# Kernel tuning notes

Measured on AMD Instinct MI355X. Metric: run time of the kernel, lower is better.

Reference implementation:

```python
import jax, jax.numpy as jnp
import numpy as np

FEAT_STRIDE = 16
SCORE_THRESH = 0.7
DIST_THRESH = 16.0
MAX_OUT = 50
B = 2048
IMG_W = 65536


def setup_inputs() -> dict:
    key = jax.random.key(0)
    k1, k2, k3 = jax.random.split(key, 3)
    fw = IMG_W // FEAT_STRIDE
    pred_cls_logit = jax.random.normal(k1, (B, fw), dtype=jnp.float32)
    pred_delta = jax.random.normal(k2, (B, fw, 2), dtype=jnp.float32)
    # realistic image widths in [0.5, 1.0] * img_width
    real_images_width = jax.random.uniform(k3, (B,), jnp.float32, 0.5, 1.0) * IMG_W
    return {
        "pred_cls_logit": pred_cls_logit,
        "pred_delta": pred_delta,
        "img_width": IMG_W,
        "real_images_width": real_images_width,
    }


def _nms_one(positions, scores):
    # positions: [N, 2], scores: [N]. Greedy 1D NMS, fixed MAX_OUT iterations.
    centers = positions.mean(axis=1)                      # [N]
    alive0 = scores >= SCORE_THRESH                       # score-threshold filter

    def step(alive, _):
        masked = jnp.where(alive, scores, -1e30)
        i = jnp.argmax(masked)                            # highest remaining score
        has = jnp.any(alive)
        f = has.astype(jnp.float32)                       # 1.0 if a box was picked
        p = positions[i] * f
        s = scores[i] * f
        # suppress everything within DIST_THRESH of picked center (incl. itself)
        new_alive = alive & (jnp.abs(centers - centers[i]) > DIST_THRESH)
        return new_alive, (p, s, f)

    _, (P, S, F) = jax.lax.scan(step, alive0, None, length=MAX_OUT)
    # pad_to_fixed_size: append validity flag column, zero-padded rows
    nms_positions = jnp.concatenate([P, F[:, None]], axis=1)   # [MAX_OUT, 3]
    nms_scores = jnp.concatenate([S[:, None], F[:, None]], axis=1)  # [MAX_OUT, 2]
    return nms_positions, nms_scores


def reference(pred_cls_logit, pred_delta, img_width, real_images_width):
    feat_width = img_width // FEAT_STRIDE
    interval_center = (jnp.arange(feat_width, dtype=jnp.float32) + 0.5) * FEAT_STRIDE
    # [B, feat_width, 2]
    pos = pred_delta * FEAT_STRIDE + interval_center[None, :, None]
    scores = jax.nn.sigmoid(pred_cls_logit)               # [B, feat_width]
    max_width = real_images_width[:, None, None] - 1.0
    pos = jnp.where(pos < 0.0, 0.0, pos)
    pos = jnp.where(pos > max_width, max_width, pos)

    nms_positions, nms_scores = jax.vmap(_nms_one)(pos, scores)

    nms_center = nms_positions[..., :2].mean(axis=2)      # [B, MAX_OUT]
    x_interval_num = jnp.floor(nms_center / FEAT_STRIDE).astype(jnp.int32)
    valid = nms_positions[..., 2] == 1.0
    idx = jnp.where(valid, x_interval_num, feat_width)    # out-of-range -> dropped
    cls_ids = jax.vmap(
        lambda ii: jnp.zeros((feat_width,), jnp.float32).at[ii].set(1.0, mode='drop')
    )(idx)                                                # [B, feat_width]
    return nms_positions, nms_scores, cls_ids
```

## Files before the change

### kernel.cpp

```cpp
#include <hip/hip_runtime.h>
#include <math.h>

#define FW 4096
#define MAX_OUT 50
#define WCAP 320
#define NSLOT 1024


__global__ __launch_bounds__(256) void essp_k1(
    const float* __restrict__ logits,
    const float* __restrict__ deltas,
    const float* __restrict__ realw,
    float* stage)
{
  __shared__ float Lx[4][WCAP];
  __shared__ int   Li[4][WCAP];
  __shared__ int   Lcnt[4];

  const int row  = blockIdx.x;
  const int tid  = threadIdx.x;
  const int lane = tid & 63;
  const int w    = tid >> 6;

  const float mw = realw[row] - 1.0f;
  const float* lgr = logits + (size_t)row * FW;
  const float* dlr = deltas + (size_t)row * (2 * FW);

  int cnt = 0;
  #pragma unroll
  for (int r = 0; r < 4; ++r) {
    const int i0 = w * 1024 + r * 256 + 4 * lane;
    const float4 lx = *(const float4*)(lgr + i0);
    const float xs[4] = {lx.x, lx.y, lx.z, lx.w};
    bool c4[4]; unsigned long long m4[4];
    #pragma unroll
    for (int e = 0; e < 4; ++e) { c4[e] = (xs[e] >= 0.846f); m4[e] = __ballot(c4[e]); }
    const unsigned long long below = (1ULL << lane) - 1ULL;
    int base = cnt + __popcll(m4[0] & below) + __popcll(m4[1] & below)
                   + __popcll(m4[2] & below) + __popcll(m4[3] & below);
    int off = 0;
    #pragma unroll
    for (int e = 0; e < 4; ++e) {
      if (c4[e]) {
        const int slot = base + off;
        if (slot < WCAP) { Lx[w][slot] = xs[e]; Li[w][slot] = i0 + e; }
        ++off;
      }
    }
    cnt += __popcll(m4[0]) + __popcll(m4[1]) + __popcll(m4[2]) + __popcll(m4[3]);
  }
  if (lane == 0) Lcnt[w] = (cnt < WCAP) ? cnt : WCAP;
  __syncthreads();

  const int c0 = Lcnt[0], c1 = Lcnt[1], c2 = Lcnt[2], c3 = Lcnt[3];
  const int p1 = c0, p2 = c0 + c1, p3 = c0 + c1 + c2;
  int nc = p3 + c3; nc = (nc < NSLOT) ? nc : NSLOT;

  float* Srow = stage + (size_t)row * FW;
  unsigned short* idxrow = (unsigned short*)(Srow + 2048);

  #pragma unroll
  for (int g0 = 0; g0 < NSLOT; g0 += 256) {
    const int g = g0 + tid;
    float score = -1e30f, cen = 0.0f;
    int idx = 0;
    if (g < nc) {
      const int wsel = (g >= p1) + (g >= p2) + (g >= p3);
      int pre = 0;
      pre = (wsel == 1) ? p1 : pre;
      pre = (wsel == 2) ? p2 : pre;
      pre = (wsel == 3) ? p3 : pre;
      const int kk = g - pre;
      const float x = (&Lx[0][0])[wsel * WCAP + kk];
      idx = (&Li[0][0])[wsel * WCAP + kk];
      const float2 d = *(const float2*)(dlr + 2 * idx);
      const float ic = ((float)idx + 0.5f) * 16.0f;
      float q0 = d.x * 16.0f + ic;
      float q1 = d.y * 16.0f + ic;
      q0 = (q0 < 0.f) ? 0.f : q0;  q0 = (q0 > mw) ? mw : q0;
      q1 = (q1 < 0.f) ? 0.f : q1;  q1 = (q1 > mw) ? mw : q1;
      cen = (q0 + q1) * 0.5f;
      const float s = (float)(1.0 / (1.0 + exp(-(double)x)));
      score = (s >= 0.7f) ? s : -1e30f;
    }
    Srow[g]        = score;
    Srow[1024 + g] = cen;
    idxrow[g]      = (unsigned short)idx;
  }
}

#define INIT1(J, SS, CE, SLOT)                                                \
  unsigned long long k##J = ((SS) >= 0.7f)                                    \
      ? ((((unsigned long long)__float_as_uint(SS)) << 11)                    \
         | (unsigned)(2047 - (SLOT)))                                         \
      : 0ULL;                                                                 \
  const float c##J = (CE);

#define M2(RK, RC, KA, CA, KB, CB)                                            \
  const bool t##RK = (KB) > (KA);                                             \
  const unsigned long long RK = t##RK ? (KB) : (KA);                          \
  const float RC = t##RK ? (CB) : (CA);

#define BSTEP(CTRL) {                                                         \
  const unsigned lo_ = (unsigned)__builtin_amdgcn_update_dpp(                 \
      (int)(unsigned)bk, (int)(unsigned)bk, CTRL, 0xF, 0xF, false);           \
  const unsigned hi_ = (unsigned)__builtin_amdgcn_update_dpp(                 \
      (int)(unsigned)(bk >> 32), (int)(unsigned)(bk >> 32), CTRL, 0xF, 0xF,   \
      false);                                                                 \
  const float oc_ = __int_as_float(__builtin_amdgcn_update_dpp(               \
      __float_as_int(bc), __float_as_int(bc), CTRL, 0xF, 0xF, false));        \
  const unsigned long long ok_ = ((unsigned long long)hi_ << 32) | lo_;       \
  const bool tb_ = ok_ > bk;                                                  \
  bk = tb_ ? ok_ : bk;  bc = tb_ ? oc_ : bc; }

#define SUP(J) {                                                              \
  const bool ts_ = fabsf(c##J - wc) <= 16.0f;                                 \
  k##J = ts_ ? 0ULL : k##J; }

__global__ __launch_bounds__(64) void essp_k2(
    const float* __restrict__ deltas,
    const float* __restrict__ realw,
    float* out_pos,
    float* out_scr,
    float* cls_all)
{
  const int row  = blockIdx.x;
  const int lane = threadIdx.x;
  const int l4   = 4 * lane;
  float* Srow = cls_all + (size_t)row * FW;

  const float4 s4a = *(const float4*)(Srow + l4);
  const float4 s4b = *(const float4*)(Srow + 256 + l4);
  const float4 s4c = *(const float4*)(Srow + 512 + l4);
  const float4 s4d = *(const float4*)(Srow + 768 + l4);
  const float4 e4a = *(const float4*)(Srow + 1024 + l4);
  const float4 e4b = *(const float4*)(Srow + 1280 + l4);
  const float4 e4c = *(const float4*)(Srow + 1536 + l4);
  const float4 e4d = *(const float4*)(Srow + 1792 + l4);

  INIT1(0,  s4a.x, e4a.x, l4 + 0)
  INIT1(1,  s4a.y, e4a.y, l4 + 1)
  INIT1(2,  s4a.z, e4a.z, l4 + 2)
  INIT1(3,  s4a.w, e4a.w, l4 + 3)
  INIT1(4,  s4b.x, e4b.x, 256 + l4 + 0)
  INIT1(5,  s4b.y, e4b.y, 256 + l4 + 1)
  INIT1(6,  s4b.z, e4b.z, 256 + l4 + 2)
  INIT1(7,  s4b.w, e4b.w, 256 + l4 + 3)
  INIT1(8,  s4c.x, e4c.x, 512 + l4 + 0)
  INIT1(9,  s4c.y, e4c.y, 512 + l4 + 1)
  INIT1(10, s4c.z, e4c.z, 512 + l4 + 2)
  INIT1(11, s4c.w, e4c.w, 512 + l4 + 3)
  INIT1(12, s4d.x, e4d.x, 768 + l4 + 0)
  INIT1(13, s4d.y, e4d.y, 768 + l4 + 1)
  INIT1(14, s4d.z, e4d.z, 768 + l4 + 2)
  INIT1(15, s4d.w, e4d.w, 768 + l4 + 3)

  int pkv = -1;
  float psv = 0.f;

  #pragma unroll 1
  for (int it = 0; it < MAX_OUT; ++it) {
    M2(ka0, ca0, k0,  c0,  k1,  c1)
    M2(ka1, ca1, k2,  c2,  k3,  c3)
    M2(ka2, ca2, k4,  c4,  k5,  c5)
    M2(ka3, ca3, k6,  c6,  k7,  c7)
    M2(ka4, ca4, k8,  c8,  k9,  c9)
    M2(ka5, ca5, k10, c10, k11, c11)
    M2(ka6, ca6, k12, c12, k13, c13)
    M2(ka7, ca7, k14, c14, k15, c15)
    M2(kb0, cb0, ka0, ca0, ka1, ca1)
    M2(kb1, cb1, ka2, ca2, ka3, ca3)
    M2(kb2, cb2, ka4, ca4, ka5, ca5)
    M2(kb3, cb3, ka6, ca6, ka7, ca7)
    M2(kc0, cc0, kb0, cb0, kb1, cb1)
    M2(kc1, cc1, kb2, cb2, kb3, cb3)
    M2(kd0, cd0, kc0, cc0, kc1, cc1)

    unsigned long long bk = kd0;
    float bc = cd0;
    BSTEP(0xB1)
    BSTEP(0x4E)
    BSTEP(0x141)
    BSTEP(0x140)
    BSTEP(0x142)
    BSTEP(0x143)

    const unsigned rhi = (unsigned)__builtin_amdgcn_readlane(
        (int)(unsigned)(bk >> 32), 63);
    const unsigned rlo = (unsigned)__builtin_amdgcn_readlane(
        (int)(unsigned)bk, 63);
    const float rc = __int_as_float(
        __builtin_amdgcn_readlane(__float_as_int(bc), 63));

    const unsigned sbits = (rhi << 21) | (rlo >> 11);
    const bool valid = sbits != 0u;
    const float wc = valid ? rc : 3.0e38f;
    if (lane == it) {
      pkv = valid ? (2047 - (int)(rlo & 0x7FFu)) : -1;
      psv = __uint_as_float(sbits);
    }
    SUP(0)  SUP(1)  SUP(2)  SUP(3)  SUP(4)  SUP(5)  SUP(6)  SUP(7)
    SUP(8)  SUP(9)  SUP(10) SUP(11) SUP(12) SUP(13) SUP(14) SUP(15)
  }

  float p0 = 0.f, p1 = 0.f;
  int ci = -1;
  if (pkv >= 0) {
    const int idx = ((const unsigned short*)(Srow + 2048))[pkv];
    const float2 d = *(const float2*)(deltas + (size_t)row * (2 * FW) + 2 * idx);
    const float mw = realw[row] - 1.0f;
    const float ic = ((float)idx + 0.5f) * 16.0f;
    p0 = d.x * 16.0f + ic;
    p1 = d.y * 16.0f + ic;
    p0 = (p0 < 0.f) ? 0.f : p0;  p0 = (p0 > mw) ? mw : p0;
    p1 = (p1 < 0.f) ? 0.f : p1;  p1 = (p1 > mw) ? mw : p1;
    ci = (int)floorf(((p0 + p1) * 0.5f) * 0.0625f);
  }
  asm volatile("s_waitcnt vmcnt(0)" ::: "memory");

  const float4 z4 = make_float4(0.f, 0.f, 0.f, 0.f);
  #pragma unroll
  for (int q = 0; q < 16; ++q)
    *(float4*)(Srow + 256 * q + l4) = z4;
  asm volatile("s_waitcnt vmcnt(0)" ::: "memory");

  float* prow = out_pos + (size_t)row * (MAX_OUT * 3);
  float* srow = out_scr + (size_t)row * (MAX_OUT * 2);
  if (lane < MAX_OUT) {
    if (pkv >= 0) {
      prow[3 * lane + 0] = p0;
      prow[3 * lane + 1] = p1;
      prow[3 * lane + 2] = 1.0f;
      srow[2 * lane + 0] = psv;
      srow[2 * lane + 1] = 1.0f;
      if (ci >= 0 && ci < FW) Srow[ci] = 1.0f;
    } else {
      prow[3 * lane + 0] = 0.0f;
      prow[3 * lane + 1] = 0.0f;
      prow[3 * lane + 2] = 0.0f;
      srow[2 * lane + 0] = 0.0f;
      srow[2 * lane + 1] = 0.0f;
    }
  }
}

extern "C" void kernel_launch(void* const* d_in, const int* in_sizes, int n_in,
                              void* d_out, int out_size, void* d_ws, size_t ws_size,
                              hipStream_t stream) {
  const float* logits = (const float*)d_in[0];
  const float* deltas = (const float*)d_in[1];
  const float* realw  = (const float*)d_in[3];
  const int Bn = in_sizes[3];
  float* out_pos = (float*)d_out;
  float* out_scr = out_pos + (size_t)Bn * MAX_OUT * 3;
  float* out_cls = out_scr + (size_t)Bn * MAX_OUT * 2;

  essp_k1<<<Bn, 256, 0, stream>>>(logits, deltas, realw, out_cls);
  essp_k2<<<Bn, 64, 0, stream>>>(deltas, realw, out_pos, out_scr, out_cls);
}
```

Before: 64.02 us.

## Prefilter top candidates by threshold bisection, run NMS on one register per lane

Before greedy NMS, the kernel bisects on the score bits with ballot counts to find a threshold that keeps between 50 and 64 candidates. It compacts those into shared memory so each lane holds one key, which removes the 16-way per-lane reduction tree and the 16 suppress compares from each of the 50 iterations. If the top 64 run out before 50 picks, it falls back to the original full-register loop, and it also exits early when nothing is left alive. The bisection adds up to 34 ballot passes per row, and rows that hit the fallback pay for both paths.

```diff
diff --git a/kernel.cpp b/kernel.cpp
--- a/kernel.cpp
+++ b/kernel.cpp
@@ -89,12 +89,27 @@
   }
 }
 
-#define INIT1(J, SS, CE, SLOT)                                                \
-  unsigned long long k##J = ((SS) >= 0.7f)                                    \
-      ? ((((unsigned long long)__float_as_uint(SS)) << 11)                    \
-         | (unsigned)(2047 - (SLOT)))                                         \
-      : 0ULL;                                                                 \
+#define KDEF(J, SS, CE)                                                       \
+  const unsigned kb##J = ((SS) >= 0.7f) ? __float_as_uint(SS) : 0u;           \
   const float c##J = (CE);
+
+#define CNT1(J) cmid += __popcll(__ballot(kb##J >= mid));
+#define ALV1(J) alive += __popcll(__ballot(kb##J != 0u));
+
+#define CPT(J, SLOTEXPR) {                                                    \
+  const unsigned long long mm_ = __ballot(kb##J >= T);                        \
+  if (kb##J >= T) {                                                           \
+    const int pos_ = nsel + __popcll(mm_ & below);                            \
+    Lkey[pos_] = (((unsigned long long)kb##J) << 11)                          \
+                 | (unsigned)(2047 - (SLOTEXPR));                             \
+    Lcen[pos_] = c##J;                                                        \
+  }                                                                           \
+  nsel += __popcll(mm_); }
+
+#define INIT1F(J, SLOTEXPR)                                                   \
+  unsigned long long fk##J = kb##J                                            \
+      ? ((((unsigned long long)kb##J) << 11) | (unsigned)(2047 - (SLOTEXPR))) \
+      : 0ULL;
 
 #define M2(RK, RC, KA, CA, KB, CB)                                            \
   const bool t##RK = (KB) > (KA);                                             \
@@ -113,9 +128,9 @@
   const bool tb_ = ok_ > bk;                                                  \
   bk = tb_ ? ok_ : bk;  bc = tb_ ? oc_ : bc; }
 
-#define SUP(J) {                                                              \
+#define SUPF(J) {                                                             \
   const bool ts_ = fabsf(c##J - wc) <= 16.0f;                                 \
-  k##J = ts_ ? 0ULL : k##J; }
+  fk##J = ts_ ? 0ULL : fk##J; }
 
 __global__ __launch_bounds__(64) void essp_k2(
     const float* __restrict__ deltas,
@@ -124,10 +139,14 @@
     float* out_scr,
     float* cls_all)
 {
+  __shared__ unsigned long long Lkey[64];
+  __shared__ float Lcen[64];
+
   const int row  = blockIdx.x;
   const int lane = threadIdx.x;
   const int l4   = 4 * lane;
   float* Srow = cls_all + (size_t)row * FW;
+  const unsigned long long below = (1ULL << lane) - 1ULL;
 
   const float4 s4a = *(const float4*)(Srow + l4);
   const float4 s4b = *(const float4*)(Srow + 256 + l4);
@@ -138,69 +157,129 @@
   const float4 e4c = *(const float4*)(Srow + 1536 + l4);
   const float4 e4d = *(const float4*)(Srow + 1792 + l4);
 
-  INIT1(0,  s4a.x, e4a.x, l4 + 0)
-  INIT1(1,  s4a.y, e4a.y, l4 + 1)
-  INIT1(2,  s4a.z, e4a.z, l4 + 2)
-  INIT1(3,  s4a.w, e4a.w, l4 + 3)
-  INIT1(4,  s4b.x, e4b.x, 256 + l4 + 0)
-  INIT1(5,  s4b.y, e4b.y, 256 + l4 + 1)
-  INIT1(6,  s4b.z, e4b.z, 256 + l4 + 2)
-  INIT1(7,  s4b.w, e4b.w, 256 + l4 + 3)
-  INIT1(8,  s4c.x, e4c.x, 512 + l4 + 0)
-  INIT1(9,  s4c.y, e4c.y, 512 + l4 + 1)
-  INIT1(10, s4c.z, e4c.z, 512 + l4 + 2)
-  INIT1(11, s4c.w, e4c.w, 512 + l4 + 3)
-  INIT1(12, s4d.x, e4d.x, 768 + l4 + 0)
-  INIT1(13, s4d.y, e4d.y, 768 + l4 + 1)
-  INIT1(14, s4d.z, e4d.z, 768 + l4 + 2)
-  INIT1(15, s4d.w, e4d.w, 768 + l4 + 3)
+  KDEF(0,  s4a.x, e4a.x)  KDEF(1,  s4a.y, e4a.y)
+  KDEF(2,  s4a.z, e4a.z)  KDEF(3,  s4a.w, e4a.w)
+  KDEF(4,  s4b.x, e4b.x)  KDEF(5,  s4b.y, e4b.y)
+  KDEF(6,  s4b.z, e4b.z)  KDEF(7,  s4b.w, e4b.w)
+  KDEF(8,  s4c.x, e4c.x)  KDEF(9,  s4c.y, e4c.y)
+  KDEF(10, s4c.z, e4c.z)  KDEF(11, s4c.w, e4c.w)
+  KDEF(12, s4d.x, e4d.x)  KDEF(13, s4d.y, e4d.y)
+  KDEF(14, s4d.z, e4d.z)  KDEF(15, s4d.w, e4d.w)
+
+  int alive = 0;
+  ALV1(0)  ALV1(1)  ALV1(2)  ALV1(3)  ALV1(4)  ALV1(5)  ALV1(6)  ALV1(7)
+  ALV1(8)  ALV1(9)  ALV1(10) ALV1(11) ALV1(12) ALV1(13) ALV1(14) ALV1(15)
+
+  bool fb = false;
+  unsigned T = 1u;
+  if (alive > 64) {
+    unsigned lo = 1u, hi = 0xFFFFFFFFu;
+    bool ok = false;
+    #pragma unroll 1
+    for (int p = 0; p < 34 && !ok; ++p) {
+      const unsigned mid = lo + ((hi - lo) >> 1);
+      int cmid = 0;
+      CNT1(0)  CNT1(1)  CNT1(2)  CNT1(3)  CNT1(4)  CNT1(5)  CNT1(6)  CNT1(7)
+      CNT1(8)  CNT1(9)  CNT1(10) CNT1(11) CNT1(12) CNT1(13) CNT1(14) CNT1(15)
+      if (cmid >= MAX_OUT && cmid <= 64) { T = mid; ok = true; }
+      else if (cmid > 64) lo = mid + 1;
+      else hi = mid - 1;
+    }
+    fb = !ok;
+  }
 
   int pkv = -1;
   float psv = 0.f;
-
-  #pragma unroll 1
-  for (int it = 0; it < MAX_OUT; ++it) {
-    M2(ka0, ca0, k0,  c0,  k1,  c1)
-    M2(ka1, ca1, k2,  c2,  k3,  c3)
-    M2(ka2, ca2, k4,  c4,  k5,  c5)
-    M2(ka3, ca3, k6,  c6,  k7,  c7)
-    M2(ka4, ca4, k8,  c8,  k9,  c9)
-    M2(ka5, ca5, k10, c10, k11, c11)
-    M2(ka6, ca6, k12, c12, k13, c13)
-    M2(ka7, ca7, k14, c14, k15, c15)
-    M2(kb0, cb0, ka0, ca0, ka1, ca1)
-    M2(kb1, cb1, ka2, ca2, ka3, ca3)
-    M2(kb2, cb2, ka4, ca4, ka5, ca5)
-    M2(kb3, cb3, ka6, ca6, ka7, ca7)
-    M2(kc0, cc0, kb0, cb0, kb1, cb1)
-    M2(kc1, cc1, kb2, cb2, kb3, cb3)
-    M2(kd0, cd0, kc0, cc0, kc1, cc1)
-
-    unsigned long long bk = kd0;
-    float bc = cd0;
-    BSTEP(0xB1)
-    BSTEP(0x4E)
-    BSTEP(0x141)
-    BSTEP(0x140)
-    BSTEP(0x142)
-    BSTEP(0x143)
-
-    const unsigned rhi = (unsigned)__builtin_amdgcn_readlane(
-        (int)(unsigned)(bk >> 32), 63);
-    const unsigned rlo = (unsigned)__builtin_amdgcn_readlane(
-        (int)(unsigned)bk, 63);
-    const float rc = __int_as_float(
-        __builtin_amdgcn_readlane(__float_as_int(bc), 63));
-
-    const unsigned sbits = (rhi << 21) | (rlo >> 11);
-    const bool valid = sbits != 0u;
-    const float wc = valid ? rc : 3.0e38f;
-    if (lane == it) {
-      pkv = valid ? (2047 - (int)(rlo & 0x7FFu)) : -1;
-      psv = __uint_as_float(sbits);
-    }
-    SUP(0)  SUP(1)  SUP(2)  SUP(3)  SUP(4)  SUP(5)  SUP(6)  SUP(7)
-    SUP(8)  SUP(9)  SUP(10) SUP(11) SUP(12) SUP(13) SUP(14) SUP(15)
+  int nsel = 0;
+
+  if (!fb) {
+    CPT(0,  l4 + 0)       CPT(1,  l4 + 1)       CPT(2,  l4 + 2)
+    CPT(3,  l4 + 3)       CPT(4,  256 + l4 + 0) CPT(5,  256 + l4 + 1)
+    CPT(6,  256 + l4 + 2) CPT(7,  256 + l4 + 3) CPT(8,  512 + l4 + 0)
+    CPT(9,  512 + l4 + 1) CPT(10, 512 + l4 + 2) CPT(11, 512 + l4 + 3)
+    CPT(12, 768 + l4 + 0) CPT(13, 768 + l4 + 1) CPT(14, 768 + l4 + 2)
+    CPT(15, 768 + l4 + 3)
+
+    unsigned long long key = (lane < nsel) ? Lkey[lane] : 0ULL;
+    float cen = (lane < nsel) ? Lcen[lane] : 0.f;
+
+    int cacc = 0;
+    #pragma unroll 1
+    for (int it = 0; it < MAX_OUT; ++it) {
+      unsigned long long bk = key;
+      float bc = cen;
+      BSTEP(0xB1)
+      BSTEP(0x4E)
+      BSTEP(0x141)
+      BSTEP(0x140)
+      BSTEP(0x142)
+      BSTEP(0x143)
+      const unsigned rhi = (unsigned)__builtin_amdgcn_readlane(
+          (int)(unsigned)(bk >> 32), 63);
+      const unsigned rlo = (unsigned)__builtin_amdgcn_readlane(
+          (int)(unsigned)bk, 63);
+      const float rc = __int_as_float(
+          __builtin_amdgcn_readlane(__float_as_int(bc), 63));
+      const unsigned sbits = (rhi << 21) | (rlo >> 11);
+      if (sbits == 0u) break;
+      if (lane == it) {
+        pkv = 2047 - (int)(rlo & 0x7FFu);
+        psv = __uint_as_float(sbits);
+      }
+      ++cacc;
+      const float wc = rc;
+      if (fabsf(cen - wc) <= 16.0f) key = 0ULL;
+    }
+    if (cacc < MAX_OUT && alive > nsel) fb = true;
+  }
+
+  if (fb) {
+    pkv = -1; psv = 0.f;
+    INIT1F(0,  l4 + 0)       INIT1F(1,  l4 + 1)       INIT1F(2,  l4 + 2)
+    INIT1F(3,  l4 + 3)       INIT1F(4,  256 + l4 + 0) INIT1F(5,  256 + l4 + 1)
+    INIT1F(6,  256 + l4 + 2) INIT1F(7,  256 + l4 + 3) INIT1F(8,  512 + l4 + 0)
+    INIT1F(9,  512 + l4 + 1) INIT1F(10, 512 + l4 + 2) INIT1F(11, 512 + l4 + 3)
+    INIT1F(12, 768 + l4 + 0) INIT1F(13, 768 + l4 + 1) INIT1F(14, 768 + l4 + 2)
+    INIT1F(15, 768 + l4 + 3)
+
+    #pragma unroll 1
+    for (int it = 0; it < MAX_OUT; ++it) {
+      M2(ka0, ca0, fk0,  c0,  fk1,  c1)
+      M2(ka1, ca1, fk2,  c2,  fk3,  c3)
+      M2(ka2, ca2, fk4,  c4,  fk5,  c5)
+      M2(ka3, ca3, fk6,  c6,  fk7,  c7)
+      M2(ka4, ca4, fk8,  c8,  fk9,  c9)
+      M2(ka5, ca5, fk10, c10, fk11, c11)
+      M2(ka6, ca6, fk12, c12, fk13, c13)
+      M2(ka7, ca7, fk14, c14, fk15, c15)
+      M2(kb0, cb0, ka0, ca0, ka1, ca1)
+      M2(kb1, cb1, ka2, ca2, ka3, ca3)
+      M2(kb2, cb2, ka4, ca4, ka5, ca5)
+      M2(kb3, cb3, ka6, ca6, ka7, ca7)
+      M2(kc0, cc0, kb0, cb0, kb1, cb1)
+      M2(kc1, cc1, kb2, cb2, kb3, cb3)
+      M2(kd0, cd0, kc0, cc0, kc1, cc1)
+
+      unsigned long long bk = kd0;
+      float bc = cd0;
+      BSTEP(0xB1) BSTEP(0x4E) BSTEP(0x141) BSTEP(0x140) BSTEP(0x142) BSTEP(0x143)
+
+      const unsigned rhi = (unsigned)__builtin_amdgcn_readlane(
+          (int)(unsigned)(bk >> 32), 63);
+      const unsigned rlo = (unsigned)__builtin_amdgcn_readlane(
+          (int)(unsigned)bk, 63);
+      const float rc = __int_as_float(
+          __builtin_amdgcn_readlane(__float_as_int(bc), 63));
+      const unsigned sbits = (rhi << 21) | (rlo >> 11);
+      const bool valid = sbits != 0u;
+      const float wc = valid ? rc : 3.0e38f;
+      if (lane == it) {
+        pkv = valid ? (2047 - (int)(rlo & 0x7FFu)) : -1;
+        psv = __uint_as_float(sbits);
+      }
+      SUPF(0)  SUPF(1)  SUPF(2)  SUPF(3)  SUPF(4)  SUPF(5)  SUPF(6)  SUPF(7)
+      SUPF(8)  SUPF(9)  SUPF(10) SUPF(11) SUPF(12) SUPF(13) SUPF(14) SUPF(15)
+    }
   }
 
   float p0 = 0.f, p1 = 0.f;
```

Result: slower. 80.29 us (+25.4%).
